# Kernel tuning notes

Measured on AMD Instinct MI355X. Metric: run time of the kernel, lower is better.

The kernel has to match this reference:

```python
import jax, jax.numpy as jnp
import numpy as np

DIM = 256
HEADS = 8
HEAD_DIM = DIM // HEADS  # 32
SCALE = HEAD_DIM ** -0.5
EPS = 1e-5


def _ternary_spike(x, vth):
    # x: [B,C,H,W], vth: [C] -> spikes in {-1,0,+1}
    v = vth[None, :, None, None]
    return jnp.where(x >= v, 1.0, 0.0) - jnp.where(x <= -v, 1.0, 0.0)


def setup_inputs() -> dict:
    key = jax.random.key(0)
    ks = jax.random.split(key, 5)
    B, C, H, W = 16, DIM, 64, 64
    s = C ** -0.5  # kaiming-ish scale for 1x1 conv weights
    return {
        "x": jax.random.normal(ks[0], (B, C, H, W), jnp.float32),
        "q_w": jax.random.normal(ks[1], (C, C), jnp.float32) * s,
        "k_w": jax.random.normal(ks[2], (C, C), jnp.float32) * s,
        "v_w": jax.random.normal(ks[3], (C, C), jnp.float32) * s,
        "proj_w": jax.random.normal(ks[4], (C, C), jnp.float32) * s,
        "bn_gamma": jnp.ones((C,), jnp.float32),
        "bn_beta": jnp.zeros((C,), jnp.float32),
        "q_vth": jnp.ones((C,), jnp.float32),
        "k_vth": jnp.ones((C,), jnp.float32),
    }


def reference(x, q_w, k_w, v_w, proj_w, bn_gamma, bn_beta, q_vth, k_vth):
    B, C, H, W = x.shape
    N = H * W
    # 1x1 convs == per-pixel channel matmuls
    q = jnp.einsum('oc,bchw->bohw', q_w, x)
    k = jnp.einsum('oc,bchw->bohw', k_w, x)
    v0 = jnp.einsum('oc,bchw->bohw', v_w, x)
    # BatchNorm2d (training-mode batch stats over B,H,W)
    mean = v0.mean(axis=(0, 2, 3))
    var = v0.var(axis=(0, 2, 3))
    v = (v0 - mean[None, :, None, None]) * jax.lax.rsqrt(var + EPS)[None, :, None, None]
    v = v * bn_gamma[None, :, None, None] + bn_beta[None, :, None, None]
    # ternary spiking activations on q, k
    qs = _ternary_spike(q, q_vth).reshape(B, HEADS, HEAD_DIM, N)
    ks_ = _ternary_spike(k, k_vth).reshape(B, HEADS, HEAD_DIM, N)
    vr = v.reshape(B, HEADS, HEAD_DIM, N)
    # channel-wise linear attention: [B,h,d,d] scores over spatial N
    attn = jax.nn.softmax(jnp.einsum('bhdn,bhen->bhde', qs, ks_) * SCALE, axis=-1)
    out = jnp.einsum('bhde,bhen->bhdn', attn, vr).reshape(B, C, H, W)
    return jnp.einsum('oc,bchw->bohw', proj_w, out) + x
```

## Files before the change

### kernel.cpp

```cpp
#include <hip/hip_runtime.h>
#include <hip/hip_bf16.h>
#include <stdint.h>
#include <math.h>

typedef __attribute__((ext_vector_type(4))) float f32x4;
typedef __attribute__((ext_vector_type(8))) short s16x8;

#define MFMA16(a,b,c) __builtin_amdgcn_mfma_f32_16x16x32_bf16((a),(b),(c),0,0,0)

#define Cc 256
#define Nc 4096
#define SCALE_F 0.17677669529663688f

__device__ __forceinline__ uint16_t f2bf(float x){
  uint32_t u = __float_as_uint(x);
  return (uint16_t)((u + 0x7fffu + ((u >> 16) & 1u)) >> 16);
}
__device__ __forceinline__ float bf2f(uint16_t b){
  return __uint_as_float(((uint32_t)b) << 16);
}

extern "C" __global__ __launch_bounds__(256) void k0_prep(
    const float* __restrict__ qw, const float* __restrict__ kw, const float* __restrict__ vw,
    uint16_t* __restrict__ qwh, uint16_t* __restrict__ qwl,
    uint16_t* __restrict__ kwh, uint16_t* __restrict__ kwl,
    uint16_t* __restrict__ vwb)
{
  int i = blockIdx.x * 256 + threadIdx.x;
  float q = qw[i]; uint16_t qh = f2bf(q);
  qwh[i] = qh; qwl[i] = f2bf(q - bf2f(qh));
  float k = kw[i]; uint16_t kh = f2bf(k);
  kwh[i] = kh; kwl[i] = f2bf(k - bf2f(kh));
  vwb[i] = f2bf(vw[i]);
}

extern "C" __global__ __launch_bounds__(256, 4) void k1_qkv(
    const float* __restrict__ x,
    const uint16_t* __restrict__ qwh, const uint16_t* __restrict__ qwl,
    const uint16_t* __restrict__ kwh, const uint16_t* __restrict__ kwl,
    const uint16_t* __restrict__ vwb,
    const float* __restrict__ qvth, const float* __restrict__ kvth,
    uint16_t* __restrict__ qs, uint16_t* __restrict__ ks,
    uint16_t* __restrict__ v0t,
    float* __restrict__ psum, float* __restrict__ psq)
{
  __shared__ __align__(16) uint16_t XS[16384];
  __shared__ float vq_s[128];
  __shared__ float vk_s[128];

  const int tid  = threadIdx.x;
  const int lane = tid & 63, wid = tid >> 6;
  const int l15  = lane & 15, lg = lane >> 4;
  const int nb = blockIdx.x, oh = blockIdx.y, b = blockIdx.z;
  const int OH = oh * 128;
  const int wrow = OH + wid * 32;
  const int nbase = nb * 32;

  if (tid < 128) vq_s[tid] = qvth[OH + tid];
  else           vk_s[tid - 128] = kvth[OH + tid - 128];

  uint16_t* XH = XS;
  uint16_t* XL = XS + 8192;

  #pragma unroll
  for (int ni_s = 0; ni_s < 2; ++ni_s){
    #pragma unroll
    for (int kst = 0; kst < 2; ++kst){
      const int n  = ni_s * 16 + l15;
      const int c0 = wid * 64 + kst * 32 + lg * 8;
      const float* xp = x + ((size_t)(b * Cc + c0)) * Nc + nbase + n;
      s16x8 vh, vl;
      #pragma unroll
      for (int j = 0; j < 8; ++j){
        float v = xp[(size_t)j * Nc];
        uint16_t h = f2bf(v);
        vh[j] = (short)h;
        vl[j] = (short)f2bf(v - bf2f(h));
      }
      const int U = ((wid * 2 + kst) * 2 + ni_s) * 64 + l15 + lg * 16;
      *(s16x8*)&XH[U * 8] = vh;
      *(s16x8*)&XL[U * 8] = vl;
    }
  }
  __syncthreads();

  const f32x4 fz = {0.f, 0.f, 0.f, 0.f};

  f32x4 accq[2][2], acck[2][2];
  #pragma unroll
  for (int mi = 0; mi < 2; ++mi)
    #pragma unroll
    for (int ni = 0; ni < 2; ++ni){ accq[mi][ni] = fz; acck[mi][ni] = fz; }

  for (int kc = 0; kc < 256; kc += 32){
    const int g = kc >> 5;
    s16x8 bh[2], bl[2];
    #pragma unroll
    for (int ni = 0; ni < 2; ++ni){
      bh[ni] = *(const s16x8*)&XH[((g * 2 + ni) * 64 + lane) * 8];
      bl[ni] = *(const s16x8*)&XL[((g * 2 + ni) * 64 + lane) * 8];
    }
    #pragma unroll
    for (int mi = 0; mi < 2; ++mi){
      const int wa = (wrow + mi * 16 + l15) * Cc + kc + lg * 8;
      s16x8 aqh = *(const s16x8*)&qwh[wa];
      s16x8 aql = *(const s16x8*)&qwl[wa];
      s16x8 akh = *(const s16x8*)&kwh[wa];
      s16x8 akl = *(const s16x8*)&kwl[wa];
      #pragma unroll
      for (int ni = 0; ni < 2; ++ni){
        accq[mi][ni] = MFMA16(aqh, bh[ni], accq[mi][ni]);
        accq[mi][ni] = MFMA16(aqh, bl[ni], accq[mi][ni]);
        accq[mi][ni] = MFMA16(aql, bh[ni], accq[mi][ni]);
        acck[mi][ni] = MFMA16(akh, bh[ni], acck[mi][ni]);
        acck[mi][ni] = MFMA16(akh, bl[ni], acck[mi][ni]);
        acck[mi][ni] = MFMA16(akl, bh[ni], acck[mi][ni]);
      }
    }
  }
  __syncthreads();

  {
    float* sscr = (float*)XL + wid * (16 * 36);
    const int o_ = lane >> 2;
    const int nloc = (lane & 3) * 8;
    #pragma unroll
    for (int mi = 0; mi < 2; ++mi){
      const int o = wrow + mi * 16 + o_;
      #pragma unroll
      for (int ni = 0; ni < 2; ++ni)
        #pragma unroll
        for (int r = 0; r < 4; ++r)
          sscr[(lg * 4 + r) * 36 + ni * 16 + l15] = accq[mi][ni][r];
      {
        const float* sp = sscr + o_ * 36 + nloc;
        const float vq = vq_s[o - OH];
        s16x8 pk;
        #pragma unroll
        for (int j = 0; j < 8; ++j){
          float v = sp[j];
          float s = (v >= vq ? 1.f : 0.f) - (v <= -vq ? 1.f : 0.f);
          pk[j] = (short)f2bf(s);
        }
        *(s16x8*)&qs[((size_t)(b * Cc + o)) * Nc + nbase + nloc] = pk;
      }
      #pragma unroll
      for (int ni = 0; ni < 2; ++ni)
        #pragma unroll
        for (int r = 0; r < 4; ++r)
          sscr[(lg * 4 + r) * 36 + ni * 16 + l15] = acck[mi][ni][r];
      {
        const float* sp = sscr + o_ * 36 + nloc;
        const float vk = vk_s[o - OH];
        s16x8 pk;
        #pragma unroll
        for (int j = 0; j < 8; ++j){
          float v = sp[j];
          float s = (v >= vk ? 1.f : 0.f) - (v <= -vk ? 1.f : 0.f);
          pk[j] = (short)f2bf(s);
        }
        *(s16x8*)&ks[((size_t)(b * Cc + o)) * Nc + nbase + nloc] = pk;
      }
    }
  }

  f32x4 accv[2][2];
  #pragma unroll
  for (int mi = 0; mi < 2; ++mi)
    #pragma unroll
    for (int ni = 0; ni < 2; ++ni) accv[mi][ni] = fz;

  for (int kc = 0; kc < 256; kc += 32){
    const int g = kc >> 5;
    s16x8 bh[2];
    #pragma unroll
    for (int ni = 0; ni < 2; ++ni)
      bh[ni] = *(const s16x8*)&XH[((g * 2 + ni) * 64 + lane) * 8];
    #pragma unroll
    for (int mi = 0; mi < 2; ++mi){
      s16x8 av = *(const s16x8*)&vwb[(wrow + mi * 16 + l15) * Cc + kc + lg * 8];
      #pragma unroll
      for (int ni = 0; ni < 2; ++ni)
        accv[mi][ni] = MFMA16(av, bh[ni], accv[mi][ni]);
    }
  }

  const int bid = b * 128 + nb;
  #pragma unroll
  for (int mi = 0; mi < 2; ++mi){
    #pragma unroll
    for (int r = 0; r < 4; ++r){
      float s1 = 0.f, s2 = 0.f;
      #pragma unroll
      for (int ni = 0; ni < 2; ++ni){
        const float v = accv[mi][ni][r];
        s1 += v; s2 += v * v;
      }
      #pragma unroll
      for (int mk = 1; mk < 16; mk <<= 1){
        s1 += __shfl_xor(s1, mk);
        s2 += __shfl_xor(s2, mk);
      }
      if (l15 == 0){
        const int o = wrow + mi * 16 + lg * 4 + r;
        psum[(size_t)o * 2048 + bid] = s1;
        psq [(size_t)o * 2048 + bid] = s2;
      }
    }
  }
  __syncthreads();

  {
    float* tscr = (float*)XS + wid * (32 * 36);
    #pragma unroll
    for (int mi = 0; mi < 2; ++mi)
      #pragma unroll
      for (int ni = 0; ni < 2; ++ni)
        #pragma unroll
        for (int r = 0; r < 4; ++r)
          tscr[(mi * 16 + lg * 4 + r) * 36 + ni * 16 + l15] = accv[mi][ni][r];
    const int n = lane >> 1, half = lane & 1;
    s16x8 o0, o1;
    #pragma unroll
    for (int k = 0; k < 8; ++k){
      o0[k] = (short)f2bf(tscr[(half * 16 + k) * 36 + n]);
      o1[k] = (short)f2bf(tscr[(half * 16 + 8 + k) * 36 + n]);
    }
    uint16_t* dst = v0t + ((size_t)(b * Nc + nbase + n)) * Cc + wrow + half * 16;
    *(s16x8*)dst = o0;
    *(s16x8*)(dst + 8) = o1;
  }
}

extern "C" __global__ __launch_bounds__(256) void k2_stats(
    const float* __restrict__ psum, const float* __restrict__ psq,
    const float* __restrict__ gamma, const float* __restrict__ beta,
    float* __restrict__ sc, float* __restrict__ sh)
{
  __shared__ float w1[4], w2[4];
  const int c = blockIdx.x;
  const int tid = threadIdx.x;
  const float* p1 = psum + (size_t)c * 2048 + tid * 8;
  const float* p2 = psq  + (size_t)c * 2048 + tid * 8;
  f32x4 a0 = *(const f32x4*)p1,  a1 = *(const f32x4*)(p1 + 4);
  f32x4 b0 = *(const f32x4*)p2,  b1 = *(const f32x4*)(p2 + 4);
  float s1 = a0[0]+a0[1]+a0[2]+a0[3] + a1[0]+a1[1]+a1[2]+a1[3];
  float s2 = b0[0]+b0[1]+b0[2]+b0[3] + b1[0]+b1[1]+b1[2]+b1[3];
  #pragma unroll
  for (int mk = 1; mk < 64; mk <<= 1){
    s1 += __shfl_xor(s1, mk);
    s2 += __shfl_xor(s2, mk);
  }
  if ((tid & 63) == 0){ w1[tid >> 6] = s1; w2[tid >> 6] = s2; }
  __syncthreads();
  if (tid == 0){
    float t1 = w1[0]+w1[1]+w1[2]+w1[3];
    float t2 = w2[0]+w2[1]+w2[2]+w2[3];
    const float inv = 1.f / 65536.f;
    const float mean = t1 * inv;
    const float var  = t2 * inv - mean * mean;
    const float s = gamma[c] * rsqrtf(var + 1e-5f);
    sc[c] = s;
    sh[c] = beta[c] - mean * s;
  }
}

extern "C" __global__ __launch_bounds__(256) void k3a_qk(
    const uint16_t* __restrict__ qs, const uint16_t* __restrict__ ks,
    float* __restrict__ Sbuf)
{
  __shared__ __align__(16) uint16_t QK[18432];
  const int h = blockIdx.x, b = blockIdx.y, ns = blockIdx.z;
  const int tid = threadIdx.x;
  const int lane = tid & 63, w = tid >> 6;

  uint16_t* qlds = QK;
  uint16_t* klds = QK + 8192;

  const f32x4 fz = {0.f, 0.f, 0.f, 0.f};
  f32x4 acc[2][2] = {{fz, fz}, {fz, fz}};
  const uint16_t* qb = qs + ((size_t)(b * Cc + h * 32)) * Nc;
  const uint16_t* kb = ks + ((size_t)(b * Cc + h * 32)) * Nc;

  const int row = tid & 31, seg = tid >> 5;
  for (int cc = 0; cc < 2; ++cc){
    const int n0 = ns * 512 + cc * 256;
    const uint16_t* qsrc = qb + (size_t)row * Nc + n0 + seg * 32;
    const uint16_t* ksrc = kb + (size_t)row * Nc + n0 + seg * 32;
    #pragma unroll
    for (int i = 0; i < 4; ++i){
      const int U = (seg * 2 + (row >> 4)) * 64 + (row & 15) + i * 16;
      *(s16x8*)&qlds[U * 8] = *(const s16x8*)(qsrc + i * 8);
      *(s16x8*)&klds[U * 8] = *(const s16x8*)(ksrc + i * 8);
    }
    __syncthreads();
    #pragma unroll
    for (int kci = 0; kci < 2; ++kci){
      const int g = w * 2 + kci;
      s16x8 a0 = *(const s16x8*)&qlds[((g * 2 + 0) * 64 + lane) * 8];
      s16x8 a1 = *(const s16x8*)&qlds[((g * 2 + 1) * 64 + lane) * 8];
      s16x8 b0 = *(const s16x8*)&klds[((g * 2 + 0) * 64 + lane) * 8];
      s16x8 b1 = *(const s16x8*)&klds[((g * 2 + 1) * 64 + lane) * 8];
      acc[0][0] = MFMA16(a0, b0, acc[0][0]);
      acc[0][1] = MFMA16(a0, b1, acc[0][1]);
      acc[1][0] = MFMA16(a1, b0, acc[1][0]);
      acc[1][1] = MFMA16(a1, b1, acc[1][1]);
    }
    __syncthreads();
  }

  float* Sp = (float*)QK;
  const int l15 = lane & 15, lg = lane >> 4;
  #pragma unroll
  for (int di = 0; di < 2; ++di)
    #pragma unroll
    for (int ei = 0; ei < 2; ++ei)
      #pragma unroll
      for (int r = 0; r < 4; ++r)
        Sp[w * 1056 + (di * 16 + lg * 4 + r) * 33 + ei * 16 + l15] = acc[di][ei][r];
  __syncthreads();
  for (int idx = tid; idx < 1024; idx += 256){
    const int d = idx >> 5, e = idx & 31;
    float s = Sp[0 * 1056 + d * 33 + e] + Sp[1 * 1056 + d * 33 + e]
            + Sp[2 * 1056 + d * 33 + e] + Sp[3 * 1056 + d * 33 + e];
    Sbuf[((size_t)(ns * 128 + b * 8 + h)) * 1024 + idx] = s;
  }
}

extern "C" __global__ __launch_bounds__(256) void k3b_sm(
    const float* __restrict__ Sbuf, const float* __restrict__ pw,
    const float* __restrict__ sc, const float* __restrict__ sh,
    uint16_t* __restrict__ Mp16, float* __restrict__ bias)
{
  __shared__ float Sf[32 * 33];
  __shared__ __align__(16) uint16_t attn_t[32 * 40];

  const int h = blockIdx.x, b = blockIdx.y;
  const int tid = threadIdx.x;
  const int lane = tid & 63, w = tid >> 6;
  const int l15 = lane & 15, lg = lane >> 4;

  for (int idx = tid; idx < 1024; idx += 256){
    float s = 0.f;
    #pragma unroll
    for (int ns = 0; ns < 8; ++ns)
      s += Sbuf[((size_t)(ns * 128 + b * 8 + h)) * 1024 + idx];
    Sf[(idx >> 5) * 33 + (idx & 31)] = s * SCALE_F;
  }
  __syncthreads();

  if (tid < 32){
    const int d = tid;
    float mx = -1e30f;
    #pragma unroll
    for (int e = 0; e < 32; ++e) mx = fmaxf(mx, Sf[d * 33 + e]);
    float p[32]; float sum = 0.f;
    #pragma unroll
    for (int e = 0; e < 32; ++e){ p[e] = expf(Sf[d * 33 + e] - mx); sum += p[e]; }
    const float inv = 1.f / sum;
    #pragma unroll
    for (int e = 0; e < 32; ++e) attn_t[e * 40 + d] = f2bf(p[e] * inv);
  }
  __syncthreads();

  s16x8 bfr[2];
  #pragma unroll
  for (int ei = 0; ei < 2; ++ei)
    bfr[ei] = *(const s16x8*)&attn_t[(ei * 16 + l15) * 40 + lg * 8];

  const f32x4 fz = {0.f, 0.f, 0.f, 0.f};
  f32x4 m[4][2];
  #pragma unroll
  for (int mi = 0; mi < 4; ++mi){
    m[mi][0] = fz; m[mi][1] = fz;
    const float* ap = pw + ((size_t)(w * 64 + mi * 16 + l15)) * Cc + h * 32 + lg * 8;
    f32x4 a0 = *(const f32x4*)ap;
    f32x4 a1 = *(const f32x4*)(ap + 4);
    s16x8 af;
    #pragma unroll
    for (int j = 0; j < 4; ++j){ af[j] = (short)f2bf(a0[j]); af[4 + j] = (short)f2bf(a1[j]); }
    #pragma unroll
    for (int ei = 0; ei < 2; ++ei)
      m[mi][ei] = MFMA16(af, bfr[ei], m[mi][ei]);
  }

  const float sc0 = sc[h * 32 + l15],      sc1 = sc[h * 32 + 16 + l15];
  const float sh0 = sh[h * 32 + l15],      sh1 = sh[h * 32 + 16 + l15];
  #pragma unroll
  for (int mi = 0; mi < 4; ++mi){
    #pragma unroll
    for (int r = 0; r < 4; ++r){
      const int o = w * 64 + mi * 16 + lg * 4 + r;
      uint16_t* mp = Mp16 + ((size_t)(b * Cc + o)) * Cc + h * 32;
      const float m0 = m[mi][0][r], m1 = m[mi][1][r];
      mp[l15]      = f2bf(m0 * sc0);
      mp[16 + l15] = f2bf(m1 * sc1);
      float bb = m0 * sh0 + m1 * sh1;
      #pragma unroll
      for (int mk = 1; mk < 16; mk <<= 1) bb += __shfl_xor(bb, mk);
      if (l15 == 0) atomicAdd(&bias[b * Cc + o], bb);
    }
  }
}

extern "C" __global__ __launch_bounds__(256, 2) void k4_proj(
    const uint16_t* __restrict__ Mp16, const uint16_t* __restrict__ v0t,
    const float* __restrict__ bias, const float* __restrict__ x,
    float* __restrict__ out)
{
  const int tid = threadIdx.x;
  const int lane = tid & 63, wid = tid >> 6;
  const int l15 = lane & 15, lg = lane >> 4;
  const int nb = blockIdx.x, b = blockIdx.y;
  const int nbase = nb * 64, wrow = wid * 64;

  const f32x4 fz = {0.f, 0.f, 0.f, 0.f};
  f32x4 acc[4][4];
  #pragma unroll
  for (int mi = 0; mi < 4; ++mi)
    #pragma unroll
    for (int ni = 0; ni < 4; ++ni) acc[mi][ni] = fz;

  for (int kc = 0; kc < 256; kc += 32){
    s16x8 bf[4];
    #pragma unroll
    for (int ni = 0; ni < 4; ++ni)
      bf[ni] = *(const s16x8*)&v0t[((size_t)(b * Nc + nbase + ni * 16 + l15)) * Cc + kc + lg * 8];
    #pragma unroll
    for (int mi = 0; mi < 4; ++mi){
      s16x8 af = *(const s16x8*)&Mp16[((size_t)(b * Cc + wrow + mi * 16 + l15)) * Cc + kc + lg * 8];
      #pragma unroll
      for (int ni = 0; ni < 4; ++ni)
        acc[mi][ni] = MFMA16(af, bf[ni], acc[mi][ni]);
    }
  }

  #pragma unroll
  for (int mi = 0; mi < 4; ++mi){
    #pragma unroll
    for (int r = 0; r < 4; ++r){
      const int o = wrow + mi * 16 + lg * 4 + r;
      const float bb = bias[b * Cc + o];
      const size_t base = ((size_t)(b * Cc + o)) * Nc + nbase;
      #pragma unroll
      for (int ni = 0; ni < 4; ++ni){
        const size_t aidx = base + ni * 16 + l15;
        out[aidx] = acc[mi][ni][r] + bb + x[aidx];
      }
    }
  }
}

extern "C" void kernel_launch(void* const* d_in, const int* in_sizes, int n_in,
                              void* d_out, int out_size, void* d_ws, size_t ws_size,
                              hipStream_t stream)
{
  (void)in_sizes; (void)n_in; (void)out_size; (void)ws_size;
  const float* x      = (const float*)d_in[0];
  const float* q_w    = (const float*)d_in[1];
  const float* k_w    = (const float*)d_in[2];
  const float* v_w    = (const float*)d_in[3];
  const float* proj_w = (const float*)d_in[4];
  const float* gamma  = (const float*)d_in[5];
  const float* beta   = (const float*)d_in[6];
  const float* q_vth  = (const float*)d_in[7];
  const float* k_vth  = (const float*)d_in[8];
  float* out = (float*)d_out;

  char* ws = (char*)d_ws;
  uint16_t* qwh = (uint16_t*)(ws + 0);
  uint16_t* qwl = (uint16_t*)(ws + 131072);
  uint16_t* kwh = (uint16_t*)(ws + 262144);
  uint16_t* kwl = (uint16_t*)(ws + 393216);
  uint16_t* vwb = (uint16_t*)(ws + 524288);
  uint16_t* v0t = (uint16_t*)(ws + 655360);
  float* psum   = (float*)(ws + 34209792);
  float* psq    = (float*)(ws + 36306944);
  float* Sbuf   = (float*)(ws + 34209792);
  float* sc     = (float*)(ws + 38404096);
  float* sh     = (float*)(ws + 38405120);
  uint16_t* Mp16= (uint16_t*)(ws + 38406144);
  float* bias   = (float*)(ws + 40503296);

  uint16_t* qs = (uint16_t*)d_out;
  uint16_t* ks = (uint16_t*)((char*)d_out + 33554432);

  hipMemsetAsync(bias, 0, 16 * 256 * sizeof(float), stream);

  k0_prep<<<256, 256, 0, stream>>>(q_w, k_w, v_w, qwh, qwl, kwh, kwl, vwb);
  k1_qkv<<<dim3(128, 2, 16), 256, 0, stream>>>(x, qwh, qwl, kwh, kwl, vwb,
                                               q_vth, k_vth, qs, ks, v0t, psum, psq);
  k2_stats<<<256, 256, 0, stream>>>(psum, psq, gamma, beta, sc, sh);
  k3a_qk<<<dim3(8, 16, 8), 256, 0, stream>>>(qs, ks, Sbuf);
  k3b_sm<<<dim3(8, 16), 256, 0, stream>>>(Sbuf, proj_w, sc, sh, Mp16, bias);
  k4_proj<<<dim3(64, 16), 256, 0, stream>>>(Mp16, v0t, bias, x, out);
}
```

Before: 367.4 us.

## Compute all QKV output channels per block to load and split x once

The QKV projection kernel is retiled. Each 512-thread block now covers all 256 output channels for 64 pixels, where before two blocks each covered 128 channels of 32 pixels. The fp32 input x is therefore read and split into bf16 hi/lo halves once instead of twice, and the BN partial-sum layout shrinks to match. The spike outputs are now written directly from MFMA accumulators as scalar 2-byte stores instead of going through an LDS transpose, which may reduce store coalescing. The doubled LDS footprint and larger block size also lower occupancy.

```diff
diff --git a/kernel.cpp b/kernel.cpp
--- a/kernel.cpp
+++ b/kernel.cpp
@@ -34,7 +34,7 @@
   vwb[i] = f2bf(vw[i]);
 }
 
-extern "C" __global__ __launch_bounds__(256, 4) void k1_qkv(
+extern "C" __global__ __launch_bounds__(512, 4) void k1_qkv(
     const float* __restrict__ x,
     const uint16_t* __restrict__ qwh, const uint16_t* __restrict__ qwl,
     const uint16_t* __restrict__ kwh, const uint16_t* __restrict__ kwl,
@@ -44,31 +44,28 @@
     uint16_t* __restrict__ v0t,
     float* __restrict__ psum, float* __restrict__ psq)
 {
-  __shared__ __align__(16) uint16_t XS[16384];
-  __shared__ float vq_s[128];
-  __shared__ float vk_s[128];
+  __shared__ __align__(16) uint16_t XS[32768];
+  __shared__ float vq_s[256];
+  __shared__ float vk_s[256];
 
   const int tid  = threadIdx.x;
   const int lane = tid & 63, wid = tid >> 6;
   const int l15  = lane & 15, lg = lane >> 4;
-  const int nb = blockIdx.x, oh = blockIdx.y, b = blockIdx.z;
-  const int OH = oh * 128;
-  const int wrow = OH + wid * 32;
-  const int nbase = nb * 32;
-
-  if (tid < 128) vq_s[tid] = qvth[OH + tid];
-  else           vk_s[tid - 128] = kvth[OH + tid - 128];
+  const int nb = blockIdx.x, b = blockIdx.y;
+  const int nbase = nb * 64;
+  const int wrow = wid * 32;
+
+  if (tid < 256) vq_s[tid] = qvth[tid];
+  else           vk_s[tid - 256] = kvth[tid - 256];
 
   uint16_t* XH = XS;
-  uint16_t* XL = XS + 8192;
-
-  #pragma unroll
-  for (int ni_s = 0; ni_s < 2; ++ni_s){
-    #pragma unroll
-    for (int kst = 0; kst < 2; ++kst){
-      const int n  = ni_s * 16 + l15;
-      const int c0 = wid * 64 + kst * 32 + lg * 8;
-      const float* xp = x + ((size_t)(b * Cc + c0)) * Nc + nbase + n;
+  uint16_t* XL = XS + 16384;
+
+  {
+    const int c0 = wid * 32 + lg * 8;
+    #pragma unroll
+    for (int ni = 0; ni < 4; ++ni){
+      const float* xp = x + ((size_t)(b * Cc + c0)) * Nc + nbase + ni * 16 + l15;
       s16x8 vh, vl;
       #pragma unroll
       for (int j = 0; j < 8; ++j){
@@ -77,7 +74,7 @@
         vh[j] = (short)h;
         vl[j] = (short)f2bf(v - bf2f(h));
       }
-      const int U = ((wid * 2 + kst) * 2 + ni_s) * 64 + l15 + lg * 16;
+      const int U = (wid * 4 + ni) * 64 + lane;
       *(s16x8*)&XH[U * 8] = vh;
       *(s16x8*)&XL[U * 8] = vl;
     }
@@ -86,29 +83,28 @@
 
   const f32x4 fz = {0.f, 0.f, 0.f, 0.f};
 
-  f32x4 accq[2][2], acck[2][2];
+  f32x4 accq[2][4], acck[2][4];
   #pragma unroll
   for (int mi = 0; mi < 2; ++mi)
     #pragma unroll
-    for (int ni = 0; ni < 2; ++ni){ accq[mi][ni] = fz; acck[mi][ni] = fz; }
-
-  for (int kc = 0; kc < 256; kc += 32){
-    const int g = kc >> 5;
-    s16x8 bh[2], bl[2];
-    #pragma unroll
-    for (int ni = 0; ni < 2; ++ni){
-      bh[ni] = *(const s16x8*)&XH[((g * 2 + ni) * 64 + lane) * 8];
-      bl[ni] = *(const s16x8*)&XL[((g * 2 + ni) * 64 + lane) * 8];
+    for (int ni = 0; ni < 4; ++ni){ accq[mi][ni] = fz; acck[mi][ni] = fz; }
+
+  for (int g = 0; g < 8; ++g){
+    s16x8 bh[4], bl[4];
+    #pragma unroll
+    for (int ni = 0; ni < 4; ++ni){
+      bh[ni] = *(const s16x8*)&XH[((g * 4 + ni) * 64 + lane) * 8];
+      bl[ni] = *(const s16x8*)&XL[((g * 4 + ni) * 64 + lane) * 8];
     }
     #pragma unroll
     for (int mi = 0; mi < 2; ++mi){
-      const int wa = (wrow + mi * 16 + l15) * Cc + kc + lg * 8;
+      const int wa = (wrow + mi * 16 + l15) * Cc + g * 32 + lg * 8;
       s16x8 aqh = *(const s16x8*)&qwh[wa];
       s16x8 aql = *(const s16x8*)&qwl[wa];
       s16x8 akh = *(const s16x8*)&kwh[wa];
       s16x8 akl = *(const s16x8*)&kwl[wa];
       #pragma unroll
-      for (int ni = 0; ni < 2; ++ni){
+      for (int ni = 0; ni < 4; ++ni){
         accq[mi][ni] = MFMA16(aqh, bh[ni], accq[mi][ni]);
         accq[mi][ni] = MFMA16(aqh, bl[ni], accq[mi][ni]);
         accq[mi][ni] = MFMA16(aql, bh[ni], accq[mi][ni]);
@@ -120,79 +116,54 @@
   }
   __syncthreads();
 
-  {
-    float* sscr = (float*)XL + wid * (16 * 36);
-    const int o_ = lane >> 2;
-    const int nloc = (lane & 3) * 8;
+  #pragma unroll
+  for (int mi = 0; mi < 2; ++mi){
+    #pragma unroll
+    for (int r = 0; r < 4; ++r){
+      const int o = wrow + mi * 16 + lg * 4 + r;
+      const float vq = vq_s[o], vk = vk_s[o];
+      uint16_t* qp = qs + ((size_t)(b * Cc + o)) * Nc + nbase;
+      uint16_t* kp = ks + ((size_t)(b * Cc + o)) * Nc + nbase;
+      #pragma unroll
+      for (int ni = 0; ni < 4; ++ni){
+        const float aq = accq[mi][ni][r];
+        const float ak = acck[mi][ni][r];
+        float sq = (aq >= vq ? 1.f : 0.f) - (aq <= -vq ? 1.f : 0.f);
+        float sk = (ak >= vk ? 1.f : 0.f) - (ak <= -vk ? 1.f : 0.f);
+        qp[ni * 16 + l15] = f2bf(sq);
+        kp[ni * 16 + l15] = f2bf(sk);
+      }
+    }
+  }
+
+  f32x4 accv[2][4];
+  #pragma unroll
+  for (int mi = 0; mi < 2; ++mi)
+    #pragma unroll
+    for (int ni = 0; ni < 4; ++ni) accv[mi][ni] = fz;
+
+  for (int g = 0; g < 8; ++g){
+    s16x8 bh[4];
+    #pragma unroll
+    for (int ni = 0; ni < 4; ++ni)
+      bh[ni] = *(const s16x8*)&XH[((g * 4 + ni) * 64 + lane) * 8];
     #pragma unroll
     for (int mi = 0; mi < 2; ++mi){
-      const int o = wrow + mi * 16 + o_;
-      #pragma unroll
-      for (int ni = 0; ni < 2; ++ni)
-        #pragma unroll
-        for (int r = 0; r < 4; ++r)
-          sscr[(lg * 4 + r) * 36 + ni * 16 + l15] = accq[mi][ni][r];
-      {
-        const float* sp = sscr + o_ * 36 + nloc;
-        const float vq = vq_s[o - OH];
-        s16x8 pk;
-        #pragma unroll
-        for (int j = 0; j < 8; ++j){
-          float v = sp[j];
-          float s = (v >= vq ? 1.f : 0.f) - (v <= -vq ? 1.f : 0.f);
-          pk[j] = (short)f2bf(s);
-        }
-        *(s16x8*)&qs[((size_t)(b * Cc + o)) * Nc + nbase + nloc] = pk;
-      }
-      #pragma unroll
-      for (int ni = 0; ni < 2; ++ni)
-        #pragma unroll
-        for (int r = 0; r < 4; ++r)
-          sscr[(lg * 4 + r) * 36 + ni * 16 + l15] = acck[mi][ni][r];
-      {
-        const float* sp = sscr + o_ * 36 + nloc;
-        const float vk = vk_s[o - OH];
-        s16x8 pk;
-        #pragma unroll
-        for (int j = 0; j < 8; ++j){
-          float v = sp[j];
-          float s = (v >= vk ? 1.f : 0.f) - (v <= -vk ? 1.f : 0.f);
-          pk[j] = (short)f2bf(s);
-        }
-        *(s16x8*)&ks[((size_t)(b * Cc + o)) * Nc + nbase + nloc] = pk;
-      }
-    }
-  }
-
-  f32x4 accv[2][2];
-  #pragma unroll
-  for (int mi = 0; mi < 2; ++mi)
-    #pragma unroll
-    for (int ni = 0; ni < 2; ++ni) accv[mi][ni] = fz;
-
-  for (int kc = 0; kc < 256; kc += 32){
-    const int g = kc >> 5;
-    s16x8 bh[2];
-    #pragma unroll
-    for (int ni = 0; ni < 2; ++ni)
-      bh[ni] = *(const s16x8*)&XH[((g * 2 + ni) * 64 + lane) * 8];
-    #pragma unroll
-    for (int mi = 0; mi < 2; ++mi){
-      s16x8 av = *(const s16x8*)&vwb[(wrow + mi * 16 + l15) * Cc + kc + lg * 8];
-      #pragma unroll
-      for (int ni = 0; ni < 2; ++ni)
+      s16x8 av = *(const s16x8*)&vwb[(wrow + mi * 16 + l15) * Cc + g * 32 + lg * 8];
+      #pragma unroll
+      for (int ni = 0; ni < 4; ++ni)
         accv[mi][ni] = MFMA16(av, bh[ni], accv[mi][ni]);
     }
   }
 
-  const int bid = b * 128 + nb;
+  const int bid = b * 64 + nb;
   #pragma unroll
   for (int mi = 0; mi < 2; ++mi){
     #pragma unroll
     for (int r = 0; r < 4; ++r){
       float s1 = 0.f, s2 = 0.f;
       #pragma unroll
-      for (int ni = 0; ni < 2; ++ni){
+      for (int ni = 0; ni < 4; ++ni){
         const float v = accv[mi][ni][r];
         s1 += v; s2 += v * v;
       }
@@ -203,32 +174,31 @@
       }
       if (l15 == 0){
         const int o = wrow + mi * 16 + lg * 4 + r;
-        psum[(size_t)o * 2048 + bid] = s1;
-        psq [(size_t)o * 2048 + bid] = s2;
-      }
-    }
-  }
-  __syncthreads();
+        psum[(size_t)o * 1024 + bid] = s1;
+        psq [(size_t)o * 1024 + bid] = s2;
+      }
+    }
+  }
 
   {
-    float* tscr = (float*)XS + wid * (32 * 36);
-    #pragma unroll
-    for (int mi = 0; mi < 2; ++mi)
-      #pragma unroll
-      for (int ni = 0; ni < 2; ++ni)
+    float* scrW = (float*)XL + wid * 1024;
+    #pragma unroll
+    for (int mi = 0; mi < 2; ++mi){
+      #pragma unroll
+      for (int ni = 0; ni < 4; ++ni)
         #pragma unroll
         for (int r = 0; r < 4; ++r)
-          tscr[(mi * 16 + lg * 4 + r) * 36 + ni * 16 + l15] = accv[mi][ni][r];
-    const int n = lane >> 1, half = lane & 1;
-    s16x8 o0, o1;
-    #pragma unroll
-    for (int k = 0; k < 8; ++k){
-      o0[k] = (short)f2bf(tscr[(half * 16 + k) * 36 + n]);
-      o1[k] = (short)f2bf(tscr[(half * 16 + 8 + k) * 36 + n]);
-    }
-    uint16_t* dst = v0t + ((size_t)(b * Nc + nbase + n)) * Cc + wrow + half * 16;
-    *(s16x8*)dst = o0;
-    *(s16x8*)(dst + 8) = o1;
+          scrW[(lg * 4 + r) * 64 + ni * 16 + l15] = accv[mi][ni][r];
+      s16x8 o0, o1;
+      #pragma unroll
+      for (int k = 0; k < 8; ++k){
+        o0[k] = (short)f2bf(scrW[k * 64 + lane]);
+        o1[k] = (short)f2bf(scrW[(8 + k) * 64 + lane]);
+      }
+      uint16_t* dst = v0t + ((size_t)(b * Nc + nbase + lane)) * Cc + wrow + mi * 16;
+      *(s16x8*)dst = o0;
+      *(s16x8*)(dst + 8) = o1;
+    }
   }
 }
 
@@ -240,12 +210,10 @@
   __shared__ float w1[4], w2[4];
   const int c = blockIdx.x;
   const int tid = threadIdx.x;
-  const float* p1 = psum + (size_t)c * 2048 + tid * 8;
-  const float* p2 = psq  + (size_t)c * 2048 + tid * 8;
-  f32x4 a0 = *(const f32x4*)p1,  a1 = *(const f32x4*)(p1 + 4);
-  f32x4 b0 = *(const f32x4*)p2,  b1 = *(const f32x4*)(p2 + 4);
-  float s1 = a0[0]+a0[1]+a0[2]+a0[3] + a1[0]+a1[1]+a1[2]+a1[3];
-  float s2 = b0[0]+b0[1]+b0[2]+b0[3] + b1[0]+b1[1]+b1[2]+b1[3];
+  f32x4 a0 = *(const f32x4*)(psum + (size_t)c * 1024 + tid * 4);
+  f32x4 b0 = *(const f32x4*)(psq  + (size_t)c * 1024 + tid * 4);
+  float s1 = a0[0] + a0[1] + a0[2] + a0[3];
+  float s2 = b0[0] + b0[1] + b0[2] + b0[3];
   #pragma unroll
   for (int mk = 1; mk < 64; mk <<= 1){
     s1 += __shfl_xor(s1, mk);
@@ -488,8 +456,8 @@
   hipMemsetAsync(bias, 0, 16 * 256 * sizeof(float), stream);
 
   k0_prep<<<256, 256, 0, stream>>>(q_w, k_w, v_w, qwh, qwl, kwh, kwl, vwb);
-  k1_qkv<<<dim3(128, 2, 16), 256, 0, stream>>>(x, qwh, qwl, kwh, kwl, vwb,
-                                               q_vth, k_vth, qs, ks, v0t, psum, psq);
+  k1_qkv<<<dim3(64, 16), 512, 0, stream>>>(x, qwh, qwl, kwh, kwl, vwb,
+                                           q_vth, k_vth, qs, ks, v0t, psum, psq);
   k2_stats<<<256, 256, 0, stream>>>(psum, psq, gamma, beta, sc, sh);
   k3a_qk<<<dim3(8, 16, 8), 256, 0, stream>>>(qs, ks, Sbuf);
   k3b_sm<<<dim3(8, 16), 256, 0, stream>>>(Sbuf, proj_w, sc, sh, Mp16, bias);
```

Measured after the change: 312.5 us. 14.9% less time.
